# Performance work log

Hardware: AMD Instinct MI355X
Metric: run time of the kernel (lower is better)

Reference implementation:

```python
import jax, jax.numpy as jnp
import numpy as np

BATCH = 1024
INPUT_DIM = 4096
HIDDEN_DIM = 4096
N_BLOCKS = 8
BLOCK_SIZE = HIDDEN_DIM // N_BLOCKS          # 512
IN_BLOCK_SIZE = INPUT_DIM // N_BLOCKS        # 512


def setup_inputs() -> dict:
    key = jax.random.key(0)
    ks = jax.random.split(key, 6)
    scale = 1.0 / np.sqrt(BLOCK_SIZE)  # torch GRUCell init: U(-1/sqrt(hidden), 1/sqrt(hidden))
    return {
        "x": jax.random.normal(ks[0], (BATCH, INPUT_DIM), dtype=jnp.float32),
        "h": jax.random.normal(ks[1], (BATCH, HIDDEN_DIM), dtype=jnp.float32),
        "W_ih": jax.random.normal(ks[2], (N_BLOCKS, 3 * BLOCK_SIZE, IN_BLOCK_SIZE), dtype=jnp.float32) * scale,
        "W_hh": jax.random.normal(ks[3], (N_BLOCKS, 3 * BLOCK_SIZE, BLOCK_SIZE), dtype=jnp.float32) * scale,
        "b_ih": jax.random.normal(ks[4], (N_BLOCKS, 3 * BLOCK_SIZE), dtype=jnp.float32) * scale,
        "b_hh": jax.random.normal(ks[5], (N_BLOCKS, 3 * BLOCK_SIZE), dtype=jnp.float32) * scale,
    }


def reference(x, h, W_ih, W_hh, b_ih, b_hh):
    B = x.shape[0]
    n, g3, ibs = W_ih.shape           # n_blocks, 3*block_size, input_block_size
    bs = W_hh.shape[2]                # block_size
    xb = x.reshape(B, n, ibs)         # (B, n_blocks, input_block_size)
    hb = h.reshape(B, n, bs)          # (B, n_blocks, block_size)
    # Block-diagonal GEMM: one grouped matmul over all blocks at once.
    gi = jnp.einsum('bni,ngi->bng', xb, W_ih) + b_ih   # (B, n, 3*bs)
    gh = jnp.einsum('bnh,ngh->bng', hb, W_hh) + b_hh   # (B, n, 3*bs)
    i_r, i_z, i_n = jnp.split(gi, 3, axis=-1)
    h_r, h_z, h_n = jnp.split(gh, 3, axis=-1)
    r = jax.nn.sigmoid(i_r + h_r)                      # reset gate
    z = jax.nn.sigmoid(i_z + h_z)                      # update gate
    n_gate = jnp.tanh(i_n + r * h_n)                   # candidate state
    new_h = n_gate + z * (hb - n_gate)                 # torch GRUCell: h' = (1-z)*n + z*h
    return new_h.reshape(B, n * bs)
```

## Files before the change

### kernel.cpp

```cpp
#include <hip/hip_runtime.h>
#include <hip/hip_bf16.h>
#include <stdint.h>

typedef short bf16x8 __attribute__((ext_vector_type(8)));
typedef float f32x16 __attribute__((ext_vector_type(16)));

static __device__ __forceinline__ short f2bf(float f) {
    __hip_bfloat16 b = __float2bfloat16(f);
    return __builtin_bit_cast(short, b);
}

__global__ __launch_bounds__(256) void wconv_kernel(const float* __restrict__ Wih,
                                                    const float* __restrict__ Whh,
                                                    short* __restrict__ Wfrag) {
    const int b = blockIdx.x;
    const int vb = (b & 7) * 768 + (b >> 3);
    const int gid = vb * 256 + threadIdx.x;
    const int lane = gid & 63;
    const int ksub = (gid >> 6) & 3;
    const int ks   = (gid >> 8) & 15;
    int s = gid >> 12;
    const int g = s % 3; s /= 3;
    const int wn = s & 1;
    const int jt = (s >> 1) & 7;
    const int nblk = s >> 4;
    const int j = jt * 64 + wn * 32 + (lane & 31);
    const int kk = ks * 64 + ksub * 16 + (lane >> 5) * 8;
    const float* src = (kk < 512)
        ? Wih + ((int64_t)nblk * 786432 + (int64_t)(g * 512 + j) * 512 + kk)
        : Whh + ((int64_t)nblk * 786432 + (int64_t)(g * 512 + j) * 512 + (kk - 512));
    const float4 a = ((const float4*)src)[0];
    const float4 bq = ((const float4*)src)[1];
    bf16x8 o;
    o[0] = f2bf(a.x); o[1] = f2bf(a.y); o[2] = f2bf(a.z); o[3] = f2bf(a.w);
    o[4] = f2bf(bq.x); o[5] = f2bf(bq.y); o[6] = f2bf(bq.z); o[7] = f2bf(bq.w);
    *(bf16x8*)(Wfrag + (size_t)gid * 8) = o;
}

__global__ __launch_bounds__(256) void aconv_kernel(const float* __restrict__ x,
                                                    const float* __restrict__ h,
                                                    short* __restrict__ Afrag) {
    const int b = blockIdx.x;
    const int n = b & 7;
    const int inner = b >> 3;
    const int rb = inner >> 4;
    const int u = inner & 15;
    const int tid = threadIdx.x;
    const int lane = tid & 63;
    const int s = u * 4 + (tid >> 6);
    const int row = rb * 32 + (lane & 31);
    const int kk = s * 16 + (lane >> 5) * 8;
    const float* src = (kk < 512)
        ? x + ((size_t)row * 4096 + n * 512 + kk)
        : h + ((size_t)row * 4096 + n * 512 + (kk - 512));
    const float4 a = ((const float4*)src)[0];
    const float4 bq = ((const float4*)src)[1];
    bf16x8 o;
    o[0] = f2bf(a.x); o[1] = f2bf(a.y); o[2] = f2bf(a.z); o[3] = f2bf(a.w);
    o[4] = f2bf(bq.x); o[5] = f2bf(bq.y); o[6] = f2bf(bq.z); o[7] = f2bf(bq.w);
    const size_t dst = ((((size_t)(rb * 8 + n) * 64 + s) * 64) + lane) * 8;
    *(bf16x8*)(Afrag + dst) = o;
}

__global__ __launch_bounds__(512, 2) void gru_kernel(
    const float* __restrict__ hst,
    const short* __restrict__ Wfrag, const short* __restrict__ Afrag,
    const float* __restrict__ b_ih, const float* __restrict__ b_hh,
    float* __restrict__ out)
{
    const int tid = threadIdx.x;
    const int nblk = blockIdx.x & 7;
    const int rr_ = blockIdx.x >> 3;
    const int bt = rr_ >> 3;
    const int jt = rr_ & 7;
    const int brow0 = bt * 256;

    const int lane = tid & 63;
    const int wave = tid >> 6;
    const int wm = wave >> 1;
    const int wn = wave & 1;
    const int l31 = lane & 31;
    const int k8 = lane >> 5;

    const int rb0 = (brow0 + wm * 64) >> 5;
    const char* ab0 = (const char*)Afrag + ((size_t)(rb0 * 8 + nblk) << 16) + (size_t)lane * 16;
    const char* ab1 = ab0 + (8 << 16);
    const char* wb = (const char*)Wfrag
        + ((size_t)((nblk * 16 + jt * 2 + wn) * 3) << 16) + (size_t)lane * 16;

    f32x16 acc_r[2] = {};
    f32x16 acc_z[2] = {};
    f32x16 acc_nx[2] = {};
    f32x16 acc_nh[2] = {};

    bf16x8 a0P, a1P, b0P, b1P, b2P;
    bf16x8 a0Q, a1Q, b0Q, b1Q, b2Q;
    bf16x8 a0R, a1R, b0R, b1R, b2R;
    bf16x8 a0S, a1S, b0S, b1S, b2S;

#define LDSET(T, s_)                                                       \
    {                                                                      \
        const int sc = (s_) > 63 ? 63 : (s_);                              \
        a0##T = *(const bf16x8*)(ab0 + (size_t)sc * 1024);                 \
        a1##T = *(const bf16x8*)(ab1 + (size_t)sc * 1024);                 \
        b0##T = *(const bf16x8*)(wb + (size_t)sc * 1024);                  \
        b1##T = *(const bf16x8*)(wb + (size_t)sc * 1024 + 65536);          \
        b2##T = *(const bf16x8*)(wb + (size_t)sc * 1024 + 131072);         \
    }

#define FMSET(T, accN)                                                             \
    {                                                                              \
        acc_r[0] = __builtin_amdgcn_mfma_f32_32x32x16_bf16(a0##T, b0##T, acc_r[0], 0, 0, 0); \
        acc_r[1] = __builtin_amdgcn_mfma_f32_32x32x16_bf16(a1##T, b0##T, acc_r[1], 0, 0, 0); \
        acc_z[0] = __builtin_amdgcn_mfma_f32_32x32x16_bf16(a0##T, b1##T, acc_z[0], 0, 0, 0); \
        acc_z[1] = __builtin_amdgcn_mfma_f32_32x32x16_bf16(a1##T, b1##T, acc_z[1], 0, 0, 0); \
        accN[0]  = __builtin_amdgcn_mfma_f32_32x32x16_bf16(a0##T, b2##T, accN[0], 0, 0, 0);  \
        accN[1]  = __builtin_amdgcn_mfma_f32_32x32x16_bf16(a1##T, b2##T, accN[1], 0, 0, 0);  \
    }

    LDSET(P, 0)
    LDSET(Q, 1)

    #pragma unroll 1
    for (int grp = 0; grp < 8; ++grp) {
        const int s = grp * 4;
        LDSET(R, s + 2) FMSET(P, acc_nx)
        LDSET(S, s + 3) FMSET(Q, acc_nx)
        LDSET(P, s + 4) FMSET(R, acc_nx)
        LDSET(Q, s + 5) FMSET(S, acc_nx)
    }
    #pragma unroll 1
    for (int grp = 8; grp < 16; ++grp) {
        const int s = grp * 4;
        LDSET(R, s + 2) FMSET(P, acc_nh)
        LDSET(S, s + 3) FMSET(Q, acc_nh)
        LDSET(P, s + 4) FMSET(R, acc_nh)
        LDSET(Q, s + 5) FMSET(S, acc_nh)
    }
#undef LDSET
#undef FMSET

    const int jb = jt * 64 + wn * 32 + l31;
    const int bb = nblk * 1536 + jb;
    const float br = b_ih[bb] + b_hh[bb];
    const float bz = b_ih[bb + 512] + b_hh[bb + 512];
    const float bnx = b_ih[bb + 1024];
    const float bnh = b_hh[bb + 1024];
    const int gcol = nblk * 512 + jb;
    #pragma unroll
    for (int m = 0; m < 2; ++m) {
        #pragma unroll
        for (int rr = 0; rr < 16; ++rr) {
            const int rowl = (rr & 3) + 8 * (rr >> 2) + 4 * k8;
            const int row = brow0 + wm * 64 + m * 32 + rowl;
            const size_t idx = (size_t)row * 4096 + gcol;
            const float sr = acc_r[m][rr] + br;
            const float sz = acc_z[m][rr] + bz;
            const float rg = 1.f / (1.f + __expf(-sr));
            const float zg = 1.f / (1.f + __expf(-sz));
            const float tin = (acc_nx[m][rr] + bnx) + rg * (acc_nh[m][rr] + bnh);
            const float e2 = __expf(-2.f * tin);
            const float ng = 2.f / (1.f + e2) - 1.f;
            const float hv = hst[idx];
            out[idx] = ng + zg * (hv - ng);
        }
    }
}

extern "C" void kernel_launch(void* const* d_in, const int* in_sizes, int n_in,
                              void* d_out, int out_size, void* d_ws, size_t ws_size,
                              hipStream_t stream) {
    (void)in_sizes; (void)n_in; (void)out_size; (void)ws_size;
    const float* x    = (const float*)d_in[0];
    const float* h    = (const float*)d_in[1];
    const float* W_ih = (const float*)d_in[2];
    const float* W_hh = (const float*)d_in[3];
    const float* b_ih = (const float*)d_in[4];
    const float* b_hh = (const float*)d_in[5];
    short* Wfrag = (short*)d_ws;
    short* Afrag = (short*)d_ws + (size_t)12 * 1024 * 1024;

    wconv_kernel<<<6144, 256, 0, stream>>>(W_ih, W_hh, Wfrag);
    aconv_kernel<<<4096, 256, 0, stream>>>(x, h, Afrag);
    gru_kernel<<<256, 512, 0, stream>>>(h, Wfrag, Afrag, b_ih, b_hh, (float*)d_out);
}
```

Baseline: 59.03 us.

## Stage weight fragments through an LDS ring buffer with async global-to-LDS loads

```diff
diff --git a/kernel.cpp b/kernel.cpp
--- a/kernel.cpp
+++ b/kernel.cpp
@@ -2,6 +2,9 @@
 #include <hip/hip_bf16.h>
 #include <stdint.h>
 
+#define G1CAST(p) ((const __attribute__((address_space(1))) void*)(p))
+#define L3CAST(p) ((__attribute__((address_space(3))) void*)(p))
+
 typedef short bf16x8 __attribute__((ext_vector_type(8)));
 typedef float f32x16 __attribute__((ext_vector_type(16)));
 
@@ -12,20 +15,19 @@
 
 __global__ __launch_bounds__(256) void wconv_kernel(const float* __restrict__ Wih,
                                                     const float* __restrict__ Whh,
-                                                    short* __restrict__ Wfrag) {
+                                                    short* __restrict__ Wstep) {
     const int b = blockIdx.x;
     const int vb = (b & 7) * 768 + (b >> 3);
     const int gid = vb * 256 + threadIdx.x;
     const int lane = gid & 63;
-    const int ksub = (gid >> 6) & 3;
-    const int ks   = (gid >> 8) & 15;
-    int s = gid >> 12;
-    const int g = s % 3; s /= 3;
-    const int wn = s & 1;
-    const int jt = (s >> 1) & 7;
-    const int nblk = s >> 4;
+    int t1 = gid >> 6;
+    const int g = t1 % 3;  t1 /= 3;
+    const int wn = t1 & 1; t1 >>= 1;
+    const int s = t1 & 63; t1 >>= 6;
+    const int jt = t1 & 7;
+    const int nblk = t1 >> 3;
     const int j = jt * 64 + wn * 32 + (lane & 31);
-    const int kk = ks * 64 + ksub * 16 + (lane >> 5) * 8;
+    const int kk = s * 16 + (lane >> 5) * 8;
     const float* src = (kk < 512)
         ? Wih + ((int64_t)nblk * 786432 + (int64_t)(g * 512 + j) * 512 + kk)
         : Whh + ((int64_t)nblk * 786432 + (int64_t)(g * 512 + j) * 512 + (kk - 512));
@@ -34,7 +36,7 @@
     bf16x8 o;
     o[0] = f2bf(a.x); o[1] = f2bf(a.y); o[2] = f2bf(a.z); o[3] = f2bf(a.w);
     o[4] = f2bf(bq.x); o[5] = f2bf(bq.y); o[6] = f2bf(bq.z); o[7] = f2bf(bq.w);
-    *(bf16x8*)(Wfrag + (size_t)gid * 8) = o;
+    *(bf16x8*)(Wstep + (size_t)gid * 8) = o;
 }
 
 __global__ __launch_bounds__(256) void aconv_kernel(const float* __restrict__ x,
@@ -62,18 +64,20 @@
     *(bf16x8*)(Afrag + dst) = o;
 }
 
-__global__ __launch_bounds__(512, 2) void gru_kernel(
+__global__ __launch_bounds__(256, 2) void gru_kernel(
     const float* __restrict__ hst,
-    const short* __restrict__ Wfrag, const short* __restrict__ Afrag,
+    const short* __restrict__ Wstep, const short* __restrict__ Afrag,
     const float* __restrict__ b_ih, const float* __restrict__ b_hh,
     float* __restrict__ out)
 {
+    __shared__ char ldsB[6][8192];
+
     const int tid = threadIdx.x;
     const int nblk = blockIdx.x & 7;
     const int rr_ = blockIdx.x >> 3;
     const int bt = rr_ >> 3;
     const int jt = rr_ & 7;
-    const int brow0 = bt * 256;
+    const int brow0 = bt * 128;
 
     const int lane = tid & 63;
     const int wave = tid >> 6;
@@ -85,60 +89,88 @@
     const int rb0 = (brow0 + wm * 64) >> 5;
     const char* ab0 = (const char*)Afrag + ((size_t)(rb0 * 8 + nblk) << 16) + (size_t)lane * 16;
     const char* ab1 = ab0 + (8 << 16);
-    const char* wb = (const char*)Wfrag
-        + ((size_t)((nblk * 16 + jt * 2 + wn) * 3) << 16) + (size_t)lane * 16;
+
+    const int d0 = wave * 2048;
+    const int ssrc0 = (d0 >= 6144) ? d0 - 6144 : d0;
+    const int ssrc1 = (d0 + 1024 >= 6144) ? d0 + 1024 - 6144 : d0 + 1024;
+    const char* wstep0 = (const char*)Wstep + (size_t)((nblk * 8 + jt) * 64) * 6144
+                       + (size_t)lane * 16;
+    const int boff = (wn * 3) * 1024 + lane * 16;
 
     f32x16 acc_r[2] = {};
     f32x16 acc_z[2] = {};
     f32x16 acc_nx[2] = {};
     f32x16 acc_nh[2] = {};
 
-    bf16x8 a0P, a1P, b0P, b1P, b2P;
-    bf16x8 a0Q, a1Q, b0Q, b1Q, b2Q;
-    bf16x8 a0R, a1R, b0R, b1R, b2R;
-    bf16x8 a0S, a1S, b0S, b1S, b2S;
-
-#define LDSET(T, s_)                                                       \
+    bf16x8 a0P, a1P, a0Q, a1Q, a0R, a1R, a0S, a1S;
+
+#define LDA(T, s_v)                                                        \
     {                                                                      \
-        const int sc = (s_) > 63 ? 63 : (s_);                              \
+        const int sc = (s_v) > 63 ? 63 : (s_v);                            \
         a0##T = *(const bf16x8*)(ab0 + (size_t)sc * 1024);                 \
         a1##T = *(const bf16x8*)(ab1 + (size_t)sc * 1024);                 \
-        b0##T = *(const bf16x8*)(wb + (size_t)sc * 1024);                  \
-        b1##T = *(const bf16x8*)(wb + (size_t)sc * 1024 + 65536);          \
-        b2##T = *(const bf16x8*)(wb + (size_t)sc * 1024 + 131072);         \
-    }
-
-#define FMSET(T, accN)                                                             \
-    {                                                                              \
-        acc_r[0] = __builtin_amdgcn_mfma_f32_32x32x16_bf16(a0##T, b0##T, acc_r[0], 0, 0, 0); \
-        acc_r[1] = __builtin_amdgcn_mfma_f32_32x32x16_bf16(a1##T, b0##T, acc_r[1], 0, 0, 0); \
-        acc_z[0] = __builtin_amdgcn_mfma_f32_32x32x16_bf16(a0##T, b1##T, acc_z[0], 0, 0, 0); \
-        acc_z[1] = __builtin_amdgcn_mfma_f32_32x32x16_bf16(a1##T, b1##T, acc_z[1], 0, 0, 0); \
-        accN[0]  = __builtin_amdgcn_mfma_f32_32x32x16_bf16(a0##T, b2##T, accN[0], 0, 0, 0);  \
-        accN[1]  = __builtin_amdgcn_mfma_f32_32x32x16_bf16(a1##T, b2##T, accN[1], 0, 0, 0);  \
-    }
-
-    LDSET(P, 0)
-    LDSET(Q, 1)
+    }
+
+    auto stageB = [&](int s, int slot) {
+        const int sc = s > 63 ? 63 : s;
+        const char* src = wstep0 + (size_t)sc * 6144;
+        char* dst = (char*)&ldsB[slot][0] + d0;
+        __builtin_amdgcn_global_load_lds(G1CAST(src + ssrc0), L3CAST(dst), 16, 0, 0);
+        __builtin_amdgcn_global_load_lds(G1CAST(src + ssrc1), L3CAST(dst + 1024), 16, 0, 0);
+    };
+
+#define ITER(C, L, accN)                                                            \
+    {                                                                               \
+        __builtin_amdgcn_s_barrier();                                               \
+        __builtin_amdgcn_sched_barrier(0);                                          \
+        stageB(s_ + 5, wslot);                                                      \
+        LDA(L, s_ + 3)                                                              \
+        __builtin_amdgcn_sched_barrier(0);                                          \
+        asm volatile("s_waitcnt vmcnt(12)" ::: "memory");                           \
+        __builtin_amdgcn_sched_barrier(0);                                          \
+        const char* bp = &ldsB[rslot][boff];                                        \
+        bf16x8 b0 = *(const bf16x8*)(bp);                                           \
+        bf16x8 b1 = *(const bf16x8*)(bp + 1024);                                    \
+        bf16x8 b2 = *(const bf16x8*)(bp + 2048);                                    \
+        __builtin_amdgcn_s_setprio(1);                                              \
+        acc_r[0] = __builtin_amdgcn_mfma_f32_32x32x16_bf16(a0##C, b0, acc_r[0], 0, 0, 0); \
+        acc_r[1] = __builtin_amdgcn_mfma_f32_32x32x16_bf16(a1##C, b0, acc_r[1], 0, 0, 0); \
+        acc_z[0] = __builtin_amdgcn_mfma_f32_32x32x16_bf16(a0##C, b1, acc_z[0], 0, 0, 0); \
+        acc_z[1] = __builtin_amdgcn_mfma_f32_32x32x16_bf16(a1##C, b1, acc_z[1], 0, 0, 0); \
+        accN[0]  = __builtin_amdgcn_mfma_f32_32x32x16_bf16(a0##C, b2, accN[0], 0, 0, 0);  \
+        accN[1]  = __builtin_amdgcn_mfma_f32_32x32x16_bf16(a1##C, b2, accN[1], 0, 0, 0);  \
+        __builtin_amdgcn_s_setprio(0);                                              \
+        rslot = (rslot == 5) ? 0 : rslot + 1;                                       \
+        wslot = (wslot == 5) ? 0 : wslot + 1;                                       \
+        s_ += 1;                                                                    \
+    }
+
+    stageB(0, 0); stageB(1, 1); stageB(2, 2); stageB(3, 3); stageB(4, 4);
+    LDA(P, 0) LDA(Q, 1) LDA(R, 2)
+    __builtin_amdgcn_sched_barrier(0);
+    asm volatile("s_waitcnt vmcnt(12)" ::: "memory");
+    __builtin_amdgcn_sched_barrier(0);
+
+    int s_ = 0;
+    int rslot = 0;
+    int wslot = 5;
 
     #pragma unroll 1
-    for (int grp = 0; grp < 8; ++grp) {
-        const int s = grp * 4;
-        LDSET(R, s + 2) FMSET(P, acc_nx)
-        LDSET(S, s + 3) FMSET(Q, acc_nx)
-        LDSET(P, s + 4) FMSET(R, acc_nx)
-        LDSET(Q, s + 5) FMSET(S, acc_nx)
+    for (int g4 = 0; g4 < 8; ++g4) {
+        ITER(P, S, acc_nx)
+        ITER(Q, P, acc_nx)
+        ITER(R, Q, acc_nx)
+        ITER(S, R, acc_nx)
     }
     #pragma unroll 1
-    for (int grp = 8; grp < 16; ++grp) {
-        const int s = grp * 4;
-        LDSET(R, s + 2) FMSET(P, acc_nh)
-        LDSET(S, s + 3) FMSET(Q, acc_nh)
-        LDSET(P, s + 4) FMSET(R, acc_nh)
-        LDSET(Q, s + 5) FMSET(S, acc_nh)
-    }
-#undef LDSET
-#undef FMSET
+    for (int g4 = 0; g4 < 8; ++g4) {
+        ITER(P, S, acc_nh)
+        ITER(Q, P, acc_nh)
+        ITER(R, Q, acc_nh)
+        ITER(S, R, acc_nh)
+    }
+#undef ITER
+#undef LDA
 
     const int jb = jt * 64 + wn * 32 + l31;
     const int bb = nblk * 1536 + jb;
@@ -177,10 +209,10 @@
     const float* W_hh = (const float*)d_in[3];
     const float* b_ih = (const float*)d_in[4];
     const float* b_hh = (const float*)d_in[5];
-    short* Wfrag = (short*)d_ws;
+    short* Wstep = (short*)d_ws;
     short* Afrag = (short*)d_ws + (size_t)12 * 1024 * 1024;
 
-    wconv_kernel<<<6144, 256, 0, stream>>>(W_ih, W_hh, Wfrag);
+    wconv_kernel<<<6144, 256, 0, stream>>>(W_ih, W_hh, Wstep);
     aconv_kernel<<<4096, 256, 0, stream>>>(x, h, Afrag);
-    gru_kernel<<<256, 512, 0, stream>>>(h, Wfrag, Afrag, b_ih, b_hh, (float*)d_out);
-}
+    gru_kernel<<<512, 256, 0, stream>>>(h, Wstep, Afrag, b_ih, b_hh, (float*)d_out);
+}
```

Measured after the change: 60.32 us. +2.2%, slower.
